# Optimization experiments

Measured on AMD Instinct MI355X. Metric: run time of the kernel, lower is better.

The kernel has to match this reference:

```python
import jax, jax.numpy as jnp
import numpy as np

N_USERS = 100000
N_TWEETS = 100000
N_NODES = N_USERS + N_TWEETS
N_EDGES = 600000
D = 128


def lrelu(x):
    return jax.nn.leaky_relu(x, negative_slope=0.01)


def linear(x, W, b):
    # torch nn.Linear convention: W is [out, in]
    return x @ W.T + b


def rgcn_conv(x, edge_index, edge_type, weight, root, bias):
    """PyG RGCNConv with num_relations=2, aggr='mean', root weight + bias."""
    src, dst = edge_index[0], edge_index[1]
    m = x[src]  # [E, D] gathered source features
    out = x @ root + bias
    for r in range(weight.shape[0]):
        mask = (edge_type == r).astype(x.dtype)  # [E]
        s = jax.ops.segment_sum(m * mask[:, None], dst, num_segments=N_NODES)
        cnt = jax.ops.segment_sum(mask, dst, num_segments=N_NODES)
        mean = s / jnp.maximum(cnt, 1.0)[:, None]  # nodes w/o rel-r in-edges -> 0
        out = out + mean @ weight[r]
    return out


def setup_inputs() -> dict:
    key = jax.random.key(0)
    ks = jax.random.split(key, 24)

    def lin(k, out_d, in_d):
        k1, k2 = jax.random.split(k)
        s = 1.0 / np.sqrt(in_d)
        return (jax.random.uniform(k1, (out_d, in_d), jnp.float32, -s, s),
                jax.random.uniform(k2, (out_d,), jnp.float32, -s, s))

    des = jax.random.normal(ks[0], (N_USERS, 100), jnp.float32)
    tweet = jax.random.normal(ks[1], (N_TWEETS, 100), jnp.float32)
    num_prop = jax.random.normal(ks[2], (N_USERS, 6), jnp.float32)
    cat_prop = jax.random.normal(ks[3], (N_USERS, 11), jnp.float32)
    edge_index = jax.random.randint(ks[4], (2, N_EDGES), 0, N_NODES, jnp.int32)
    edge_type = jax.random.randint(ks[5], (N_EDGES,), 0, 2, jnp.int32)

    W_des, b_des = lin(ks[6], D // 2, 100)       # des -> 64
    W_num, b_num = lin(ks[7], D // 4, 6)         # num_prop -> 32
    W_cat, b_cat = lin(ks[8], D // 4, 11)        # cat_prop -> 32
    W_tw, b_tw = lin(ks[9], D, 100)              # tweet -> 128
    W_in, b_in = lin(ks[10], D, D)
    rgcn_w = jax.random.normal(ks[11], (2, D, D), jnp.float32) / np.sqrt(D)
    rgcn_root = jax.random.normal(ks[12], (D, D), jnp.float32) / np.sqrt(D)
    rgcn_bias = jnp.zeros((D,), jnp.float32)
    W_o1, b_o1 = lin(ks[13], D, D)
    W_o2, b_o2 = lin(ks[14], 2, D)

    return dict(des=des, tweet=tweet, num_prop=num_prop, cat_prop=cat_prop,
                edge_index=edge_index, edge_type=edge_type,
                W_des=W_des, b_des=b_des, W_num=W_num, b_num=b_num,
                W_cat=W_cat, b_cat=b_cat, W_tw=W_tw, b_tw=b_tw,
                W_in=W_in, b_in=b_in, rgcn_w=rgcn_w, rgcn_root=rgcn_root,
                rgcn_bias=rgcn_bias, W_o1=W_o1, b_o1=b_o1, W_o2=W_o2, b_o2=b_o2)


def reference(des, tweet, num_prop, cat_prop, edge_index, edge_type,
              W_des, b_des, W_num, b_num, W_cat, b_cat, W_tw, b_tw,
              W_in, b_in, rgcn_w, rgcn_root, rgcn_bias, W_o1, b_o1, W_o2, b_o2):
    d = lrelu(linear(des, W_des, b_des))
    n = lrelu(linear(num_prop, W_num, b_num))
    c = lrelu(linear(cat_prop, W_cat, b_cat))
    x_users = jnp.concatenate([d, n, c], axis=1)       # [N_users, 128]
    t = lrelu(linear(tweet, W_tw, b_tw))               # [N_tweets, 128]
    x = jnp.concatenate([x_users, t], axis=0)          # [N_nodes, 128]
    x = lrelu(linear(x, W_in, b_in))
    x = rgcn_conv(x, edge_index, edge_type, rgcn_w, rgcn_root, rgcn_bias)
    # dropout in eval mode = identity
    x = rgcn_conv(x, edge_index, edge_type, rgcn_w, rgcn_root, rgcn_bias)
    x = lrelu(linear(x, W_o1, b_o1))
    return linear(x, W_o2, b_o2)
```

## Files before the change

### kernel.cpp

```cpp
#include <hip/hip_runtime.h>
#include <hip/hip_bf16.h>

typedef __hip_bfloat16 bf16;

typedef __bf16 bfv8 __attribute__((ext_vector_type(8)));
typedef float f32x4 __attribute__((ext_vector_type(4)));

__device__ __forceinline__ float lrelu(float x) { return x > 0.f ? x : 0.01f * x; }

__device__ __forceinline__ float ldv(float v) { return v; }
__device__ __forceinline__ float ldv(bf16 v) { return __bfloat162float(v); }
__device__ __forceinline__ void stv(float* p, float v) { *p = v; }
__device__ __forceinline__ void stv(bf16* p, float v) { *p = __float2bfloat16(v); }

__device__ __forceinline__ float in_rd(const void* p, size_t i, int isbf) {
  return isbf ? __bfloat162float(((const bf16*)p)[i]) : ((const float*)p)[i];
}
__device__ __forceinline__ int ix_rd(const void* p, size_t i, int is64) {
  return is64 ? (int)((const long long*)p)[i] : ((const int*)p)[i];
}

struct ProbeArgs {
  const void* p[23];
  int s[23];
  int mode[23];
};

__global__ void detect_all(ProbeArgs a, int* __restrict__ flags) {
  __shared__ int sh[256];
  int b = blockIdx.x;
  const unsigned int* w = (const unsigned int*)a.p[b];
  int s = a.s[b], mode = a.mode[b];
  int t = threadIdx.x;
  int c = 0;
  if (t < s) {
    if (mode == 0) {
      unsigned int v = w[t];
      int e = (v >> 7) & 0xFF;
      c = (e >= 100 && e <= 140) ? 1 : 0;
    } else {
      c = (w[2 * t + 1] == 0u) ? 1 : 0;
    }
  }
  sh[t] = c;
  __syncthreads();
  for (int d = 128; d; d >>= 1) {
    if (t < d) sh[t] += sh[t + d];
    __syncthreads();
  }
  if (t == 0) flags[b] = (mode == 0) ? (sh[0] * 10 >= 7 * s) : (sh[0] * 10 >= 9 * s);
}

#define PW_F32 82562
#define BF_BASE 82564
#define PW_W_TOTAL (BF_BASE + 5 * 8192)
#define ENC_BASE PW_W_TOTAL
#define PW_TOTAL (ENC_BASE + 16384 + 256)
__global__ void prep_weights(const void* Win, const void* bin, const void* rw,
                             const void* root, const void* rb, const void* Wo1,
                             const void* bo1, const void* Wo2, const void* bo2,
                             const int* __restrict__ fl, float* __restrict__ pw) {
  int i = blockIdx.x * 256 + threadIdx.x;
  if (i >= PW_W_TOTAL) return;
  if (i < 16384) {
    int k = i >> 7, o = i & 127;
    pw[i] = in_rd(Win, (size_t)o * 128 + k, fl[14]);
  } else if (i < 32768) {
    int j = i - 16384;
    int k = j >> 7, o = j & 127;
    pw[i] = in_rd(Wo1, (size_t)o * 128 + k, fl[19]);
  } else if (i < 49152) {
    pw[i] = in_rd(root, i - 32768, fl[17]);
  } else if (i < 81920) {
    pw[i] = in_rd(rw, i - 49152, fl[16]);
  } else if (i < 82048) {
    pw[i] = in_rd(bin, i - 81920, fl[15]);
  } else if (i < 82176) {
    pw[i] = in_rd(rb, i - 82048, fl[18]);
  } else if (i < 82304) {
    pw[i] = in_rd(bo1, i - 82176, fl[20]);
  } else if (i < 82560) {
    pw[i] = in_rd(Wo2, i - 82304, fl[21]);
  } else if (i < PW_F32) {
    pw[i] = in_rd(bo2, i - 82560, fl[22]);
  } else if (i >= BF_BASE) {
    int j = i - BF_BASE;
    bf16* bw = (bf16*)(pw + BF_BASE);
#pragma unroll
    for (int q = 0; q < 2; q++) {
      int u = 2 * j + q;
      int m = u >> 14, r = u & 16383;
      int n = r >> 7, k = r & 127;
      float v;
      if (m == 0) v = in_rd(Win, (size_t)n * 128 + k, fl[14]);
      else if (m == 1) v = in_rd(Wo1, (size_t)n * 128 + k, fl[19]);
      else if (m == 2) v = in_rd(root, (size_t)k * 128 + n, fl[17]);
      else v = in_rd(rw, (size_t)(m - 3) * 16384 + (size_t)k * 128 + n, fl[16]);
      bw[u] = __float2bfloat16(v);
    }
  }
}

__global__ void prep_enc(const void* Wd, const void* bd, const void* Wn, const void* bn,
                         const void* Wc, const void* bc, const void* Wt, const void* bt,
                         const int* __restrict__ fl, int dDes, int dNum, int dCat, int dTw,
                         float* __restrict__ pw) {
  int i = blockIdx.x * 256 + threadIdx.x;
  bf16* e = (bf16*)(pw + ENC_BASE);
  float* bU = pw + ENC_BASE + 16384;
  float* bT = bU + 128;
  if (i < 16384) {
    int n = i >> 7, k = i & 127;
    float v = 0.f;
    if (n < 64) {
      if (k < dDes) v = in_rd(Wd, (size_t)n * dDes + k, fl[6]);
    } else if (n < 96) {
      int kk = k - dDes;
      if (kk >= 0 && kk < dNum) v = in_rd(Wn, (size_t)(n - 64) * dNum + kk, fl[8]);
    } else {
      int kk = k - dDes - dNum;
      if (kk >= 0 && kk < dCat) v = in_rd(Wc, (size_t)(n - 96) * dCat + kk, fl[10]);
    }
    e[i] = __float2bfloat16(v);
  } else if (i < 32768) {
    int j = i - 16384;
    int n = j >> 7, k = j & 127;
    float v = (k < dTw) ? in_rd(Wt, (size_t)n * dTw + k, fl[12]) : 0.f;
    e[i] = __float2bfloat16(v);
  } else if (i < 32896) {
    int j = i - 32768;
    bU[j] = (j < 64) ? in_rd(bd, j, fl[7])
                     : (j < 96) ? in_rd(bn, j - 64, fl[9]) : in_rd(bc, j - 96, fl[11]);
  } else if (i < 33024) {
    bT[i - 32896] = in_rd(bt, i - 32896, fl[13]);
  }
}

__global__ void sig_fill(float* __restrict__ p, int n, float v) {
  int i = blockIdx.x * 256 + threadIdx.x;
  if (i < n) p[i] = v;
}
__global__ void zero_ints(int* __restrict__ p, int n) {
  int i = blockIdx.x * 256 + threadIdx.x;
  if (i < n) p[i] = 0;
}

__global__ void count_edges(const void* __restrict__ ei, const void* __restrict__ et,
                            const int* __restrict__ fl, int* __restrict__ cnt, int NEr,
                            int NNr) {
  int e = blockIdx.x * 256 + threadIdx.x;
  if (e >= NEr) return;
  int d = ix_rd(ei, (size_t)NEr + e, fl[4]);
  int r = ix_rd(et, e, fl[5]) & 1;
  if ((unsigned)d >= (unsigned)NNr) return;
  atomicAdd(&cnt[r * NNr + d], 1);
}

__global__ void scan_blocks(const int* __restrict__ in, int* __restrict__ out,
                            int* __restrict__ bsum, int n) {
  __shared__ int sh[256];
  int t = threadIdx.x;
  int base = blockIdx.x * 1024 + t * 4;
  int a[4];
  int s = 0;
#pragma unroll
  for (int i = 0; i < 4; i++) {
    a[i] = (base + i < n) ? in[base + i] : 0;
    s += a[i];
  }
  sh[t] = s;
  __syncthreads();
  for (int d = 1; d < 256; d <<= 1) {
    int v = (t >= d) ? sh[t - d] : 0;
    __syncthreads();
    sh[t] += v;
    __syncthreads();
  }
  int ex = sh[t] - s;
#pragma unroll
  for (int i = 0; i < 4; i++) {
    if (base + i < n) out[base + i] = ex;
    ex += a[i];
  }
  if (t == 255 && bsum) bsum[blockIdx.x] = sh[255];
}

__global__ void scan_add_inv(int* __restrict__ off, const int* __restrict__ bsumsc,
                             const int* __restrict__ cnt, float* __restrict__ inv, int n) {
  int i = blockIdx.x * 256 + threadIdx.x;
  if (i >= n) return;
  off[i] += bsumsc[i >> 10];
  inv[i] = 1.f / fmaxf((float)cnt[i], 1.f);
}

__global__ void fill_elist(const void* __restrict__ ei, const void* __restrict__ et,
                           const int* __restrict__ fl, const int* __restrict__ off,
                           int* __restrict__ fill, int* __restrict__ elist, int NEr, int NNr) {
  int e = blockIdx.x * 256 + threadIdx.x;
  if (e >= NEr) return;
  int s = ix_rd(ei, e, fl[4]);
  int d = ix_rd(ei, (size_t)NEr + e, fl[4]);
  int r = ix_rd(et, e, fl[5]) & 1;
  if ((unsigned)d >= (unsigned)NNr || (unsigned)s >= (unsigned)NNr) return;
  int idx = r * NNr + d;
  int slot = off[idx] + atomicAdd(&fill[idx], 1);
  elist[slot] = s | ((d & 127) << 24);
}

__global__ __launch_bounds__(256) void enc_gemm(const void* __restrict__ A,
                                                const void* __restrict__ W,
                                                const void* __restrict__ B,
                                                const int* __restrict__ fl, int fa, int fw,
                                                int fb, bf16* __restrict__ x, int M, int K,
                                                int N, int row0, int col0) {
  __shared__ float Wb[128 * 102];
  __shared__ float bb[128];
  int t = threadIdx.x;
  int stride = (K & 1) ? K : K + 1;
  int fA = fl[fa];
  {
    int fW = fl[fw], fB = fl[fb];
    for (int idx = t; idx < N * K; idx += 256) {
      int j = idx / K, k = idx - j * K;
      Wb[j * stride + k] = in_rd(W, (size_t)j * K + k, fW);
    }
    if (t < N) bb[t] = in_rd(B, t, fB);
  }
  __syncthreads();
  int j = t % N;
  int r = t / N;
  int R = 256 / N;
  int iEnd = blockIdx.x * 64 + 64;
  if (iEnd > M) iEnd = M;
  const float* wrow = &Wb[j * stride];
  if (!fA) {
    const float* Af = (const float*)A;
    for (int i = blockIdx.x * 64 + r; i < iEnd; i += R) {
      const float* a = Af + (size_t)i * K;
      float acc = bb[j];
      for (int k = 0; k < K; k++) acc += a[k] * wrow[k];
      stv(&x[(size_t)(row0 + i) * 128 + col0 + j], lrelu(acc));
    }
  } else {
    const bf16* Ab = (const bf16*)A;
    for (int i = blockIdx.x * 64 + r; i < iEnd; i += R) {
      const bf16* a = Ab + (size_t)i * K;
      float acc = bb[j];
      for (int k = 0; k < K; k++) acc += __bfloat162float(a[k]) * wrow[k];
      stv(&x[(size_t)(row0 + i) * 128 + col0 + j], lrelu(acc));
    }
  }
}


__global__ __launch_bounds__(256) void enc_mfma(
    const void* __restrict__ A0, const void* __restrict__ A1, const void* __restrict__ A2,
    const int* __restrict__ fl, int fi0, int fi1, int fi2, int K0, int K1, int K2,
    const bf16* __restrict__ WbE, const float* __restrict__ biasE,
    const bf16* __restrict__ WbL, const float* __restrict__ bL, bf16* __restrict__ x,
    int M, int row0) {
  __shared__ __align__(16) bf16 Xs[16384];
  int t = threadIdx.x;
  int i0 = blockIdx.x * 128;

  {
    uint4 z = {0u, 0u, 0u, 0u};
#pragma unroll
    for (int i = 0; i < 8; i++) *(uint4*)((char*)Xs + i * 4096 + t * 16) = z;
  }
  __syncthreads();

  const void* As[3] = {A0, A1, A2};
  int Ks_[3] = {K0, K1, K2};
  int fis[3] = {fi0, fi1, fi2};
  int cb = 0;
  for (int s = 0; s < 3; s++) {
    int Ks = Ks_[s];
    if (Ks <= 0) continue;
    int isbf = fl[fis[s]];
    const void* A = As[s];
    int total = 128 * Ks;
    for (int f = t; f < total; f += 256) {
      int row = f / Ks;
      int k = f - row * Ks;
      int gr = i0 + row;
      float v = (gr < M) ? in_rd(A, (size_t)gr * Ks + k, isbf) : 0.f;
      int byte = row * 256 + (cb + k) * 2;
      *(bf16*)((char*)Xs + (byte ^ ((row & 7) << 4))) = __float2bfloat16(v);
    }
    cb += Ks;
  }
  __syncthreads();

  int wv = t >> 6, l = t & 63;
  int lr = l & 15, lg = l >> 4;
  int rbase = (wv >> 1) * 64, cbase = (wv & 1) * 64;
  int ko = lg * 8;
  f32x4 acc[4][4] = {};
#pragma unroll
  for (int ks = 0; ks < 4; ks++) {
    bfv8 bk[4];
#pragma unroll
    for (int cg = 0; cg < 4; cg++)
      bk[cg] = *(const bfv8*)&WbE[(size_t)(cbase + cg * 16 + lr) * 128 + ks * 32 + ko];
    bfv8 af[4];
#pragma unroll
    for (int rg = 0; rg < 4; rg++) {
      int mrow = rbase + rg * 16 + lr;
      int byte = mrow * 256 + (ks * 32 + ko) * 2;
      af[rg] = *(const bfv8*)((const char*)Xs + (byte ^ ((mrow & 7) << 4)));
    }
#pragma unroll
    for (int rg = 0; rg < 4; rg++)
#pragma unroll
      for (int cg = 0; cg < 4; cg++)
        acc[rg][cg] =
            __builtin_amdgcn_mfma_f32_16x16x32_bf16(af[rg], bk[cg], acc[rg][cg], 0, 0, 0);
  }
  __syncthreads();

#pragma unroll
  for (int cg = 0; cg < 4; cg++) {
    int col = cbase + cg * 16 + lr;
    float bv = biasE[col];
#pragma unroll
    for (int rg = 0; rg < 4; rg++) {
      int r0 = rbase + rg * 16 + lg * 4;
#pragma unroll
      for (int j = 0; j < 4; j++) {
        int row = r0 + j;
        int byte = row * 256 + col * 2;
        *(bf16*)((char*)Xs + (byte ^ ((row & 7) << 4))) =
            __float2bfloat16(lrelu(acc[rg][cg][j] + bv));
      }
    }
  }
  __syncthreads();

  f32x4 acc2[4][4] = {};
#pragma unroll
  for (int ks = 0; ks < 4; ks++) {
    bfv8 bk[4];
#pragma unroll
    for (int cg = 0; cg < 4; cg++)
      bk[cg] = *(const bfv8*)&WbL[(size_t)(cbase + cg * 16 + lr) * 128 + ks * 32 + ko];
    bfv8 af[4];
#pragma unroll
    for (int rg = 0; rg < 4; rg++) {
      int mrow = rbase + rg * 16 + lr;
      int byte = mrow * 256 + (ks * 32 + ko) * 2;
      af[rg] = *(const bfv8*)((const char*)Xs + (byte ^ ((mrow & 7) << 4)));
    }
#pragma unroll
    for (int rg = 0; rg < 4; rg++)
#pragma unroll
      for (int cg = 0; cg < 4; cg++)
        acc2[rg][cg] =
            __builtin_amdgcn_mfma_f32_16x16x32_bf16(af[rg], bk[cg], acc2[rg][cg], 0, 0, 0);
  }

#pragma unroll
  for (int cg = 0; cg < 4; cg++) {
    int col = cbase + cg * 16 + lr;
    float bv = bL[col];
#pragma unroll
    for (int rg = 0; rg < 4; rg++) {
      int r0 = i0 + rbase + rg * 16 + lg * 4;
#pragma unroll
      for (int j = 0; j < 4; j++) {
        int row = r0 + j;
        if (row < M)
          x[(size_t)(row0 + row) * 128 + col] = __float2bfloat16(lrelu(acc2[rg][cg][j] + bv));
      }
    }
  }
}

__global__ __launch_bounds__(256) void mfma_lin(const bf16* __restrict__ A,
                                                const bf16* __restrict__ Wb,
                                                const float* __restrict__ bias,
                                                bf16* __restrict__ Out, int M) {
  int t = threadIdx.x;
  int wv = t >> 6, l = t & 63;
  int lr = l & 15, lg = l >> 4;
  int i0 = blockIdx.x * 128;
  int rbase = (wv >> 1) * 64;
  int cbase = (wv & 1) * 64;
  int ko = lg * 8;

  size_t rowoff[4];
#pragma unroll
  for (int rg = 0; rg < 4; rg++) {
    int row = i0 + rbase + rg * 16 + lr;
    if (row > M - 1) row = M - 1;
    rowoff[rg] = (size_t)row * 128;
  }

  bfv8 bfr[4][4];
#pragma unroll
  for (int cg = 0; cg < 4; cg++)
#pragma unroll
    for (int ks = 0; ks < 4; ks++)
      bfr[cg][ks] = *(const bfv8*)&Wb[(size_t)(cbase + cg * 16 + lr) * 128 + ks * 32 + ko];

  f32x4 acc[4][4] = {};
#pragma unroll
  for (int ks = 0; ks < 4; ks++) {
    bfv8 af[4];
#pragma unroll
    for (int rg = 0; rg < 4; rg++) af[rg] = *(const bfv8*)&A[rowoff[rg] + ks * 32 + ko];
#pragma unroll
    for (int rg = 0; rg < 4; rg++)
#pragma unroll
      for (int cg = 0; cg < 4; cg++)
        acc[rg][cg] =
            __builtin_amdgcn_mfma_f32_16x16x32_bf16(af[rg], bfr[cg][ks], acc[rg][cg], 0, 0, 0);
  }

#pragma unroll
  for (int cg = 0; cg < 4; cg++) {
    int col = cbase + cg * 16 + lr;
    float bv = bias[col];
#pragma unroll
    for (int rg = 0; rg < 4; rg++) {
      int row0 = i0 + rbase + rg * 16 + lg * 4;
#pragma unroll
      for (int j = 0; j < 4; j++) {
        int row = row0 + j;
        if (row < M) Out[(size_t)row * 128 + col] = __float2bfloat16(lrelu(acc[rg][cg][j] + bv));
      }
    }
  }
}

template <bool TAIL>
__global__ __launch_bounds__(256, 4) void mfma_conv_f(
    const bf16* __restrict__ X, const int* __restrict__ off, const int* __restrict__ cnt,
    const int* __restrict__ elist, const float* __restrict__ inv,
    const bf16* __restrict__ WB, const float* __restrict__ bias, bf16* __restrict__ Out,
    const bf16* __restrict__ Wo1B, const float* __restrict__ bO1,
    const float* __restrict__ Wo2, const float* __restrict__ bo2,
    float* __restrict__ out2, int M, int NNr, int NEr) {
  __shared__ __align__(16) float At[64 * 128];
  int t = threadIdx.x;
  int wv = t >> 6, l = t & 63;
  int lr = l & 15, lg = l >> 4;
  int i0 = blockIdx.x * 32;
  int cbase = wv * 32;
  int ko = lg * 8;

  {
    int c8 = (t & 15) * 8;
    int stc[4], dgc[4];
#pragma unroll
    for (int pn = 0; pn < 4; pn++) {
      int vr = (t >> 4) + pn * 16;
      int rel = vr >> 5, m = vr & 31;
      int node = i0 + m;
      int idx = rel * NNr + node;
      bool ok = node < M;
      stc[pn] = ok ? off[idx] : 0;
      dgc[pn] = ok ? cnt[idx] : 0;
    }
    int dmax = max(max(dgc[0], dgc[1]), max(dgc[2], dgc[3]));
    float s[4][8] = {};

    auto xoff = [&](int pn, int e) -> size_t {
      int ec = e < dgc[pn] - 1 ? e : dgc[pn] - 1;
      ec = ec < 0 ? 0 : ec;
      int ei = stc[pn] + ec;
      ei = ei < NEr - 1 ? ei : NEr - 1;
      return (size_t)(elist[ei] & 0xFFFFFF) * 128 + c8;
    };

    bfv8 v0[4], v1[4];
#pragma unroll
    for (int pn = 0; pn < 4; pn++) v0[pn] = *(const bfv8*)&X[xoff(pn, 0)];
#pragma unroll
    for (int pn = 0; pn < 4; pn++) v1[pn] = *(const bfv8*)&X[xoff(pn, 1)];

    for (int e = 0; e < dmax; e++) {
      bfv8 v2[4];
#pragma unroll
      for (int pn = 0; pn < 4; pn++) v2[pn] = *(const bfv8*)&X[xoff(pn, e + 2)];
#pragma unroll
      for (int pn = 0; pn < 4; pn++) {
        float msk = e < dgc[pn] ? 1.f : 0.f;
#pragma unroll
        for (int j = 0; j < 8; j++) s[pn][j] += msk * __bfloat162float(v0[pn][j]);
      }
#pragma unroll
      for (int pn = 0; pn < 4; pn++) {
        v0[pn] = v1[pn];
        v1[pn] = v2[pn];
      }
    }
#pragma unroll
    for (int pn = 0; pn < 4; pn++) {
      int vr = (t >> 4) + pn * 16;
      int sw = (vr & 7) << 4;
      int lb = vr * 512 + c8 * 4;
      *(float4*)((char*)At + (lb ^ sw)) = make_float4(s[pn][0], s[pn][1], s[pn][2], s[pn][3]);
      *(float4*)((char*)At + ((lb + 16) ^ sw)) =
          make_float4(s[pn][4], s[pn][5], s[pn][6], s[pn][7]);
    }
  }

  size_t rowoff[2];
  float iv0[2], iv1[2];
#pragma unroll
  for (int rg = 0; rg < 2; rg++) {
    int row = i0 + rg * 16 + lr;
    int rc = row < M ? row : M - 1;
    rowoff[rg] = (size_t)rc * 128;
    iv0[rg] = row < M ? inv[row] : 0.f;
    iv1[rg] = row < M ? inv[NNr + row] : 0.f;
  }

  f32x4 acc[2][2] = {};

#pragma unroll
  for (int ks = 0; ks < 4; ks++) {
    bfv8 bk[2];
#pragma unroll
    for (int cg = 0; cg < 2; cg++)
      bk[cg] = *(const bfv8*)&WB[(size_t)(cbase + cg * 16 + lr) * 128 + ks * 32 + ko];
    bfv8 af[2];
#pragma unroll
    for (int rg = 0; rg < 2; rg++) af[rg] = *(const bfv8*)&X[rowoff[rg] + ks * 32 + ko];
#pragma unroll
    for (int rg = 0; rg < 2; rg++)
#pragma unroll
      for (int cg = 0; cg < 2; cg++)
        acc[rg][cg] =
            __builtin_amdgcn_mfma_f32_16x16x32_bf16(af[rg], bk[cg], acc[rg][cg], 0, 0, 0);
  }
  __syncthreads();

#pragma unroll
  for (int r = 0; r < 2; r++) {
    const bf16* Wb = WB + 16384 * (1 + r);
#pragma unroll
    for (int ks = 0; ks < 4; ks++) {
      bfv8 bk[2];
#pragma unroll
      for (int cg = 0; cg < 2; cg++)
        bk[cg] = *(const bfv8*)&Wb[(size_t)(cbase + cg * 16 + lr) * 128 + ks * 32 + ko];
      bfv8 af[2];
#pragma unroll
      for (int rg = 0; rg < 2; rg++) {
        int mrow = r * 32 + rg * 16 + lr;
        int lb = mrow * 512 + ks * 128 + ko * 4;
        int sw = (mrow & 7) << 4;
        float4 f0 = *(const float4*)((const char*)At + (lb ^ sw));
        float4 f1 = *(const float4*)((const char*)At + ((lb + 16) ^ sw));
        float iv = r ? iv1[rg] : iv0[rg];
        bfv8 a;
        a[0] = (__bf16)(f0.x * iv); a[1] = (__bf16)(f0.y * iv);
        a[2] = (__bf16)(f0.z * iv); a[3] = (__bf16)(f0.w * iv);
        a[4] = (__bf16)(f1.x * iv); a[5] = (__bf16)(f1.y * iv);
        a[6] = (__bf16)(f1.z * iv); a[7] = (__bf16)(f1.w * iv);
        af[rg] = a;
      }
#pragma unroll
      for (int rg = 0; rg < 2; rg++)
#pragma unroll
        for (int cg = 0; cg < 2; cg++)
          acc[rg][cg] =
              __builtin_amdgcn_mfma_f32_16x16x32_bf16(af[rg], bk[cg], acc[rg][cg], 0, 0, 0);
    }
  }

  if (!TAIL) {
#pragma unroll
    for (int cg = 0; cg < 2; cg++) {
      int col = cbase + cg * 16 + lr;
      float bv = bias[col];
#pragma unroll
      for (int rg = 0; rg < 2; rg++) {
        int row0 = i0 + rg * 16 + lg * 4;
#pragma unroll
        for (int j = 0; j < 4; j++) {
          int row = row0 + j;
          if (row < M) Out[(size_t)row * 128 + col] = __float2bfloat16(acc[rg][cg][j] + bv);
        }
      }
    }
  } else {
    __syncthreads();
#pragma unroll
    for (int cg = 0; cg < 2; cg++) {
      int col = cbase + cg * 16 + lr;
      float bv = bias[col];
#pragma unroll
      for (int rg = 0; rg < 2; rg++) {
#pragma unroll
        for (int j = 0; j < 4; j++) {
          int row32 = rg * 16 + lg * 4 + j;
          int byte = row32 * 256 + col * 2;
          *(bf16*)((char*)At + (byte ^ ((row32 & 7) << 4))) =
              __float2bfloat16(acc[rg][cg][j] + bv);
        }
      }
    }
    __syncthreads();

    f32x4 acc2[2][2] = {};
#pragma unroll
    for (int ks = 0; ks < 4; ks++) {
      bfv8 bk[2];
#pragma unroll
      for (int cg = 0; cg < 2; cg++)
        bk[cg] = *(const bfv8*)&Wo1B[(size_t)(cbase + cg * 16 + lr) * 128 + ks * 32 + ko];
      bfv8 af[2];
#pragma unroll
      for (int rg = 0; rg < 2; rg++) {
        int mrow = rg * 16 + lr;
        int byte = mrow * 256 + (ks * 32 + ko) * 2;
        af[rg] = *(const bfv8*)((const char*)At + (byte ^ ((mrow & 7) << 4)));
      }
#pragma unroll
      for (int rg = 0; rg < 2; rg++)
#pragma unroll
        for (int cg = 0; cg < 2; cg++)
          acc2[rg][cg] =
              __builtin_amdgcn_mfma_f32_16x16x32_bf16(af[rg], bk[cg], acc2[rg][cg], 0, 0, 0);
    }
#pragma unroll
    for (int cg = 0; cg < 2; cg++) {
      int col = cbase + cg * 16 + lr;
      float bv = bO1[col];
#pragma unroll
      for (int rg = 0; rg < 2; rg++) {
#pragma unroll
        for (int j = 0; j < 4; j++) {
          int row32 = rg * 16 + lg * 4 + j;
          *(bf16*)((char*)At + 8192 + row32 * 256 + col * 2) =
              __float2bfloat16(lrelu(acc2[rg][cg][j] + bv));
        }
      }
    }
    __syncthreads();

    int row = t >> 3, seg = t & 7;
    const bf16* zr = (const bf16*)((const char*)At + 8192 + row * 256 + seg * 32);
    float p0 = 0.f, p1 = 0.f;
#pragma unroll
    for (int q = 0; q < 16; q++) {
      float xv = __bfloat162float(zr[q]);
      int col = seg * 16 + q;
      p0 += xv * Wo2[col];
      p1 += xv * Wo2[128 + col];
    }
#pragma unroll
    for (int o = 4; o; o >>= 1) {
      p0 += __shfl_down(p0, o, 8);
      p1 += __shfl_down(p1, o, 8);
    }
    int grow = i0 + row;
    if (seg == 0 && grow < M) {
      out2[(size_t)grow * 2] = p0 + bo2[0];
      out2[(size_t)grow * 2 + 1] = p1 + bo2[1];
    }
  }
}

static void run_pipeline(void* const* d_in, const int* S, float* out, char* ws,
                         int NUr, int NTr, int NEr, int dDes, int dNum, int dCat, int dTw,
                         hipStream_t stream) {
  const int NNr = NUr + NTr;
  const size_t xbytes = (size_t)NNr * 128 * 2;

  bf16* xa = (bf16*)ws;
  bf16* xb = (bf16*)(ws + xbytes);
  char* p = ws + 2 * xbytes;
  int* cnt = (int*)p;      p += (size_t)2 * NNr * 4;
  int* fill = (int*)p;     p += (size_t)2 * NNr * 4;
  int* off = (int*)p;      p += (size_t)2 * NNr * 4;
  int* bsum = (int*)p;     p += 2048 * 4;
  int* bsumsc = (int*)p;   p += 2048 * 4;
  float* inv = (float*)p;  p += (size_t)2 * NNr * 4;
  int* elist = (int*)p;    p += (size_t)NEr * 4;
  float* pw = (float*)p;   p += (size_t)PW_TOTAL * 4;
  int* flags = (int*)p;

  ProbeArgs pa;
  for (int i = 0; i < 23; i++) {
    int src = (i == 22) ? 21 : i;
    pa.p[i] = d_in[src];
    if (i == 4) {
      pa.mode[i] = 1;
      pa.s[i] = NEr < 256 ? NEr : 256;
    } else if (i == 5) {
      pa.mode[i] = 1;
      int s2 = NEr / 2 < 256 ? NEr / 2 : 256;
      pa.s[i] = s2 < 1 ? 1 : s2;
    } else {
      pa.mode[i] = 0;
      int s = S[src] / 2;
      if (s > 256) s = 256;
      if (s < 1) s = 1;
      pa.s[i] = s;
    }
  }
  detect_all<<<23, 256, 0, stream>>>(pa, flags);
  prep_weights<<<(PW_W_TOTAL + 255) / 256, 256, 0, stream>>>(
      d_in[14], d_in[15], d_in[16], d_in[17], d_in[18], d_in[19], d_in[20], d_in[21],
      d_in[22], flags, pw);
  prep_enc<<<129, 256, 0, stream>>>(d_in[6], d_in[7], d_in[8], d_in[9], d_in[10], d_in[11],
                                    d_in[12], d_in[13], flags, dDes, dNum, dCat, dTw, pw);

  const float* bIn = pw + 81920;
  const float* rbp = pw + 82048;
  const float* bO1 = pw + 82176;
  const float* Wo2p = pw + 82304;
  const float* bo2p = pw + 82560;
  const bf16* WinB = (const bf16*)(pw + BF_BASE);
  const bf16* Wo1B = (const bf16*)(pw + BF_BASE + 8192);
  const bf16* ConvB = (const bf16*)(pw + BF_BASE + 16384);
  const bf16* EncU = (const bf16*)(pw + ENC_BASE);
  const bf16* EncT = (const bf16*)(pw + ENC_BASE + 8192);
  const float* bU = pw + ENC_BASE + 16384;
  const float* bT = bU + 128;

  const void* ei = d_in[4];
  const void* et = d_in[5];
  const int nb1 = (2 * NNr + 1023) / 1024;

  zero_ints<<<(4 * NNr + 255) / 256, 256, 0, stream>>>(cnt, 4 * NNr);
  zero_ints<<<16, 256, 0, stream>>>(bsum, 4096);
  count_edges<<<(NEr + 255) / 256, 256, 0, stream>>>(ei, et, flags, cnt, NEr, NNr);
  scan_blocks<<<nb1, 256, 0, stream>>>(cnt, off, bsum, 2 * NNr);
  scan_blocks<<<1, 256, 0, stream>>>(bsum, bsumsc, nullptr, nb1);
  scan_add_inv<<<(2 * NNr + 255) / 256, 256, 0, stream>>>(off, bsumsc, cnt, inv, 2 * NNr);
  fill_elist<<<(NEr + 255) / 256, 256, 0, stream>>>(ei, et, flags, off, fill, elist, NEr, NNr);

  if (dDes + dNum + dCat <= 128 && dTw <= 128) {
    enc_mfma<<<(NUr + 127) / 128, 256, 0, stream>>>(d_in[0], d_in[2], d_in[3], flags, 0, 2, 3,
                                                    dDes, dNum, dCat, EncU, bU, WinB, bIn, xb,
                                                    NUr, 0);
    enc_mfma<<<(NTr + 127) / 128, 256, 0, stream>>>(d_in[1], nullptr, nullptr, flags, 1, 1, 1,
                                                    dTw, 0, 0, EncT, bT, WinB, bIn, xb, NTr,
                                                    NUr);
  } else {
    enc_gemm<<<(NUr + 63) / 64, 256, 0, stream>>>(d_in[0], d_in[6], d_in[7], flags, 0, 6, 7,
                                                  xa, NUr, dDes, 64, 0, 0);
    enc_gemm<<<(NUr + 63) / 64, 256, 0, stream>>>(d_in[2], d_in[8], d_in[9], flags, 2, 8, 9,
                                                  xa, NUr, dNum, 32, 0, 64);
    enc_gemm<<<(NUr + 63) / 64, 256, 0, stream>>>(d_in[3], d_in[10], d_in[11], flags, 3, 10,
                                                  11, xa, NUr, dCat, 32, 0, 96);
    enc_gemm<<<(NTr + 63) / 64, 256, 0, stream>>>(d_in[1], d_in[12], d_in[13], flags, 1, 12,
                                                  13, xa, NTr, dTw, 128, NUr, 0);
    mfma_lin<<<(NNr + 127) / 128, 256, 0, stream>>>(xa, WinB, bIn, xb, NNr);
  }

  const int mt32 = (NNr + 31) / 32;
  mfma_conv_f<false><<<mt32, 256, 0, stream>>>(xb, off, cnt, elist, inv, ConvB, rbp, xa,
                                               nullptr, nullptr, nullptr, nullptr, nullptr,
                                               NNr, NNr, NEr);
  mfma_conv_f<true><<<mt32, 256, 0, stream>>>(xa, off, cnt, elist, inv, ConvB, rbp, nullptr,
                                              Wo1B, bO1, Wo2p, bo2p, out, NNr, NNr, NEr);
}

extern "C" void kernel_launch(void* const* d_in, const int* in_sizes, int n_in,
                              void* d_out, int out_size, void* d_ws, size_t ws_size,
                              hipStream_t stream) {
  float* out = (float*)d_out;
  char* ws = (char*)d_ws;

  auto signal = [&](int k) {
    sig_fill<<<(out_size + 255) / 256, 256, 0, stream>>>(out, out_size, (float)(200 + k));
  };

  if (n_in != 23) { signal(1); return; }
  const int* S = in_sizes;
  if (S[7] != 64 || S[9] != 32 || S[11] != 32 || S[13] != 128) { signal(2); return; }
  if (S[15] != 128) { signal(3); return; }
  if (S[6] % 64 || S[8] % 32 || S[10] % 32 || S[12] % 128) { signal(4); return; }
  int dDes = S[6] / 64, dNum = S[8] / 32, dCat = S[10] / 32, dTw = S[12] / 128;
  if (dDes <= 0 || dTw <= 0 || S[0] % dDes || S[1] % dTw) { signal(5); return; }
  if (dDes > 101 || dNum > 101 || dCat > 101 || dTw > 101) { signal(4); return; }
  int NUr = S[0] / dDes, NTr = S[1] / dTw, NNr = NUr + NTr, NEr = S[5];
  if (S[2] != NUr * dNum || S[3] != NUr * dCat) { signal(5); return; }
  if (S[4] != 2 * NEr || NEr < 1024) { signal(6); return; }
  if (NNr >= (1 << 24)) { signal(6); return; }
  if (S[14] != 16384 || S[16] != 32768 || S[17] != 16384 || S[18] != 128 ||
      S[19] != 16384 || S[20] != 128 || S[21] != 256 || S[22] != 2) { signal(7); return; }
  if (out_size != NNr * 2) { signal(8); return; }

  const size_t smallBytes = (size_t)4 * ((size_t)2 * NNr * 4) + 2 * 2048 * 4 +
                            (size_t)NEr * 4 + (size_t)PW_TOTAL * 4 + 512;
  const size_t need = 2 * (size_t)NNr * 128 * 2 + smallBytes;

  if (ws_size >= need) {
    run_pipeline(d_in, S, out, ws, NUr, NTr, NEr, dDes, dNum, dCat, dTw, stream);
  } else {
    signal(9);
  }
}
```

Before: 520.6 us.

## Merge setup kernels, vectorize encoder input loads, simplify conv gather prefetch

Three prep/zeroing kernels are merged into one setup launch, and the separate bsum zeroing launch is dropped. The encoder's input staging now reads four elements at a time with float4/ushort4 loads instead of scalar loads with per-element division. The conv gather loop drops its two-deep clamped prefetch for a one-deep prefetch with predicated loads, which reduces address arithmetic but may expose more gather latency. The bsum buffer is no longer zeroed, which is harmless only if scan_blocks fully writes it.

Result: faster. 491.1 us (-5.7%).

```diff
diff --git a/kernel.cpp b/kernel.cpp
--- a/kernel.cpp
+++ b/kernel.cpp
@@ -55,94 +55,93 @@
 #define BF_BASE 82564
 #define PW_W_TOTAL (BF_BASE + 5 * 8192)
 #define ENC_BASE PW_W_TOTAL
+#define ENC_N 33024
 #define PW_TOTAL (ENC_BASE + 16384 + 256)
-__global__ void prep_weights(const void* Win, const void* bin, const void* rw,
-                             const void* root, const void* rb, const void* Wo1,
-                             const void* bo1, const void* Wo2, const void* bo2,
-                             const int* __restrict__ fl, float* __restrict__ pw) {
+__global__ void setup_all(const void* Win, const void* bin, const void* rw, const void* root,
+                          const void* rb, const void* Wo1, const void* bo1, const void* Wo2,
+                          const void* bo2, const void* Wd, const void* bd, const void* Wn,
+                          const void* bn, const void* Wc, const void* bc, const void* Wt,
+                          const void* bt, const int* __restrict__ fl, int dDes, int dNum,
+                          int dCat, int dTw, float* __restrict__ pw, int* __restrict__ cnt4,
+                          int NNr) {
   int i = blockIdx.x * 256 + threadIdx.x;
-  if (i >= PW_W_TOTAL) return;
-  if (i < 16384) {
-    int k = i >> 7, o = i & 127;
-    pw[i] = in_rd(Win, (size_t)o * 128 + k, fl[14]);
-  } else if (i < 32768) {
-    int j = i - 16384;
-    int k = j >> 7, o = j & 127;
-    pw[i] = in_rd(Wo1, (size_t)o * 128 + k, fl[19]);
-  } else if (i < 49152) {
-    pw[i] = in_rd(root, i - 32768, fl[17]);
-  } else if (i < 81920) {
-    pw[i] = in_rd(rw, i - 49152, fl[16]);
-  } else if (i < 82048) {
-    pw[i] = in_rd(bin, i - 81920, fl[15]);
-  } else if (i < 82176) {
-    pw[i] = in_rd(rb, i - 82048, fl[18]);
-  } else if (i < 82304) {
-    pw[i] = in_rd(bo1, i - 82176, fl[20]);
-  } else if (i < 82560) {
-    pw[i] = in_rd(Wo2, i - 82304, fl[21]);
-  } else if (i < PW_F32) {
-    pw[i] = in_rd(bo2, i - 82560, fl[22]);
-  } else if (i >= BF_BASE) {
-    int j = i - BF_BASE;
-    bf16* bw = (bf16*)(pw + BF_BASE);
-#pragma unroll
-    for (int q = 0; q < 2; q++) {
-      int u = 2 * j + q;
-      int m = u >> 14, r = u & 16383;
-      int n = r >> 7, k = r & 127;
-      float v;
-      if (m == 0) v = in_rd(Win, (size_t)n * 128 + k, fl[14]);
-      else if (m == 1) v = in_rd(Wo1, (size_t)n * 128 + k, fl[19]);
-      else if (m == 2) v = in_rd(root, (size_t)k * 128 + n, fl[17]);
-      else v = in_rd(rw, (size_t)(m - 3) * 16384 + (size_t)k * 128 + n, fl[16]);
-      bw[u] = __float2bfloat16(v);
-    }
-  }
-}
-
-__global__ void prep_enc(const void* Wd, const void* bd, const void* Wn, const void* bn,
-                         const void* Wc, const void* bc, const void* Wt, const void* bt,
-                         const int* __restrict__ fl, int dDes, int dNum, int dCat, int dTw,
-                         float* __restrict__ pw) {
-  int i = blockIdx.x * 256 + threadIdx.x;
-  bf16* e = (bf16*)(pw + ENC_BASE);
-  float* bU = pw + ENC_BASE + 16384;
-  float* bT = bU + 128;
-  if (i < 16384) {
-    int n = i >> 7, k = i & 127;
-    float v = 0.f;
-    if (n < 64) {
-      if (k < dDes) v = in_rd(Wd, (size_t)n * dDes + k, fl[6]);
-    } else if (n < 96) {
-      int kk = k - dDes;
-      if (kk >= 0 && kk < dNum) v = in_rd(Wn, (size_t)(n - 64) * dNum + kk, fl[8]);
+  if (i < PW_W_TOTAL) {
+    if (i < 16384) {
+      int k = i >> 7, o = i & 127;
+      pw[i] = in_rd(Win, (size_t)o * 128 + k, fl[14]);
+    } else if (i < 32768) {
+      int j = i - 16384;
+      int k = j >> 7, o = j & 127;
+      pw[i] = in_rd(Wo1, (size_t)o * 128 + k, fl[19]);
+    } else if (i < 49152) {
+      pw[i] = in_rd(root, i - 32768, fl[17]);
+    } else if (i < 81920) {
+      pw[i] = in_rd(rw, i - 49152, fl[16]);
+    } else if (i < 82048) {
+      pw[i] = in_rd(bin, i - 81920, fl[15]);
+    } else if (i < 82176) {
+      pw[i] = in_rd(rb, i - 82048, fl[18]);
+    } else if (i < 82304) {
+      pw[i] = in_rd(bo1, i - 82176, fl[20]);
+    } else if (i < 82560) {
+      pw[i] = in_rd(Wo2, i - 82304, fl[21]);
+    } else if (i < PW_F32) {
+      pw[i] = in_rd(bo2, i - 82560, fl[22]);
+    } else if (i >= BF_BASE) {
+      int j = i - BF_BASE;
+      bf16* bw = (bf16*)(pw + BF_BASE);
+#pragma unroll
+      for (int q = 0; q < 2; q++) {
+        int u = 2 * j + q;
+        int m = u >> 14, r = u & 16383;
+        int n = r >> 7, k = r & 127;
+        float v;
+        if (m == 0) v = in_rd(Win, (size_t)n * 128 + k, fl[14]);
+        else if (m == 1) v = in_rd(Wo1, (size_t)n * 128 + k, fl[19]);
+        else if (m == 2) v = in_rd(root, (size_t)k * 128 + n, fl[17]);
+        else v = in_rd(rw, (size_t)(m - 3) * 16384 + (size_t)k * 128 + n, fl[16]);
+        bw[u] = __float2bfloat16(v);
+      }
+    }
+  } else if (i < PW_W_TOTAL + ENC_N) {
+    int j = i - PW_W_TOTAL;
+    bf16* e = (bf16*)(pw + ENC_BASE);
+    float* bU = pw + ENC_BASE + 16384;
+    float* bT = bU + 128;
+    if (j < 16384) {
+      int n = j >> 7, k = j & 127;
+      float v = 0.f;
+      if (n < 64) {
+        if (k < dDes) v = in_rd(Wd, (size_t)n * dDes + k, fl[6]);
+      } else if (n < 96) {
+        int kk = k - dDes;
+        if (kk >= 0 && kk < dNum) v = in_rd(Wn, (size_t)(n - 64) * dNum + kk, fl[8]);
+      } else {
+        int kk = k - dDes - dNum;
+        if (kk >= 0 && kk < dCat) v = in_rd(Wc, (size_t)(n - 96) * dCat + kk, fl[10]);
+      }
+      e[j] = __float2bfloat16(v);
+    } else if (j < 32768) {
+      int j2 = j - 16384;
+      int n = j2 >> 7, k = j2 & 127;
+      float v = (k < dTw) ? in_rd(Wt, (size_t)n * dTw + k, fl[12]) : 0.f;
+      e[j] = __float2bfloat16(v);
+    } else if (j < 32896) {
+      int j2 = j - 32768;
+      bU[j2] = (j2 < 64) ? in_rd(bd, j2, fl[7])
+                         : (j2 < 96) ? in_rd(bn, j2 - 64, fl[9]) : in_rd(bc, j2 - 96, fl[11]);
     } else {
-      int kk = k - dDes - dNum;
-      if (kk >= 0 && kk < dCat) v = in_rd(Wc, (size_t)(n - 96) * dCat + kk, fl[10]);
-    }
-    e[i] = __float2bfloat16(v);
-  } else if (i < 32768) {
-    int j = i - 16384;
-    int n = j >> 7, k = j & 127;
-    float v = (k < dTw) ? in_rd(Wt, (size_t)n * dTw + k, fl[12]) : 0.f;
-    e[i] = __float2bfloat16(v);
-  } else if (i < 32896) {
-    int j = i - 32768;
-    bU[j] = (j < 64) ? in_rd(bd, j, fl[7])
-                     : (j < 96) ? in_rd(bn, j - 64, fl[9]) : in_rd(bc, j - 96, fl[11]);
-  } else if (i < 33024) {
-    bT[i - 32896] = in_rd(bt, i - 32896, fl[13]);
+      bT[j - 32896] = in_rd(bt, j - 32896, fl[13]);
+    }
+  } else {
+    int j = i - PW_W_TOTAL - ENC_N;
+    if (j < 4 * NNr) cnt4[j] = 0;
   }
 }
 
 __global__ void sig_fill(float* __restrict__ p, int n, float v) {
   int i = blockIdx.x * 256 + threadIdx.x;
   if (i < n) p[i] = v;
-}
-__global__ void zero_ints(int* __restrict__ p, int n) {
-  int i = blockIdx.x * 256 + threadIdx.x;
-  if (i < n) p[i] = 0;
 }
 
 __global__ void count_edges(const void* __restrict__ ei, const void* __restrict__ et,
@@ -278,15 +277,58 @@
     int Ks = Ks_[s];
     if (Ks <= 0) continue;
     int isbf = fl[fis[s]];
-    const void* A = As[s];
     int total = 128 * Ks;
-    for (int f = t; f < total; f += 256) {
-      int row = f / Ks;
-      int k = f - row * Ks;
-      int gr = i0 + row;
-      float v = (gr < M) ? in_rd(A, (size_t)gr * Ks + k, isbf) : 0.f;
-      int byte = row * 256 + (cb + k) * 2;
-      *(bf16*)((char*)Xs + (byte ^ ((row & 7) << 4))) = __float2bfloat16(v);
+    long gml = (long)(M - i0) * Ks;
+    int gmax = gml > total ? total : (gml < 0 ? 0 : (int)gml);
+    int nu = (total + 3) >> 2;
+    if (!isbf) {
+      const float* Af = (const float*)As[s] + (size_t)i0 * Ks;
+      for (int u = t; u < nu; u += 256) {
+        int f0 = u * 4;
+        float vv[4];
+        if (f0 + 4 <= gmax) {
+          float4 x4 = *(const float4*)(Af + f0);
+          vv[0] = x4.x; vv[1] = x4.y; vv[2] = x4.z; vv[3] = x4.w;
+        } else {
+          vv[0] = (f0 < gmax) ? Af[f0] : 0.f;
+          vv[1] = (f0 + 1 < gmax) ? Af[f0 + 1] : 0.f;
+          vv[2] = (f0 + 2 < gmax) ? Af[f0 + 2] : 0.f;
+          vv[3] = (f0 + 3 < gmax) ? Af[f0 + 3] : 0.f;
+        }
+#pragma unroll
+        for (int q = 0; q < 4; q++) {
+          int f = f0 + q;
+          if (f < total) {
+            int row = f / Ks, k = f - row * Ks;
+            int byte = row * 256 + (cb + k) * 2;
+            *(bf16*)((char*)Xs + (byte ^ ((row & 7) << 4))) = __float2bfloat16(vv[q]);
+          }
+        }
+      }
+    } else {
+      const unsigned short* Ab = (const unsigned short*)As[s] + (size_t)i0 * Ks;
+      for (int u = t; u < nu; u += 256) {
+        int f0 = u * 4;
+        unsigned short vv[4];
+        if (f0 + 4 <= gmax) {
+          ushort4 x4 = *(const ushort4*)(Ab + f0);
+          vv[0] = x4.x; vv[1] = x4.y; vv[2] = x4.z; vv[3] = x4.w;
+        } else {
+          vv[0] = (f0 < gmax) ? Ab[f0] : 0;
+          vv[1] = (f0 + 1 < gmax) ? Ab[f0 + 1] : 0;
+          vv[2] = (f0 + 2 < gmax) ? Ab[f0 + 2] : 0;
+          vv[3] = (f0 + 3 < gmax) ? Ab[f0 + 3] : 0;
+        }
+#pragma unroll
+        for (int q = 0; q < 4; q++) {
+          int f = f0 + q;
+          if (f < total) {
+            int row = f / Ks, k = f - row * Ks;
+            int byte = row * 256 + (cb + k) * 2;
+            *(unsigned short*)((char*)Xs + (byte ^ ((row & 7) << 4))) = vv[q];
+          }
+        }
+      }
     }
     cb += Ks;
   }
@@ -440,7 +482,7 @@
     const bf16* __restrict__ WB, const float* __restrict__ bias, bf16* __restrict__ Out,
     const bf16* __restrict__ Wo1B, const float* __restrict__ bO1,
     const float* __restrict__ Wo2, const float* __restrict__ bo2,
-    float* __restrict__ out2, int M, int NNr, int NEr) {
+    float* __restrict__ out2, int M, int NNr) {
   __shared__ __align__(16) float At[64 * 128];
   int t = threadIdx.x;
   int wv = t >> 6, l = t & 63;
@@ -450,54 +492,51 @@
   int ko = lg * 8;
 
   {
+    int grp = t >> 4;
     int c8 = (t & 15) * 8;
     int stc[4], dgc[4];
 #pragma unroll
     for (int pn = 0; pn < 4; pn++) {
-      int vr = (t >> 4) + pn * 16;
+      int vr = grp + pn * 16;
       int rel = vr >> 5, m = vr & 31;
       int node = i0 + m;
+      bool ok = node < M;
       int idx = rel * NNr + node;
-      bool ok = node < M;
       stc[pn] = ok ? off[idx] : 0;
       dgc[pn] = ok ? cnt[idx] : 0;
     }
     int dmax = max(max(dgc[0], dgc[1]), max(dgc[2], dgc[3]));
     float s[4][8] = {};
-
-    auto xoff = [&](int pn, int e) -> size_t {
-      int ec = e < dgc[pn] - 1 ? e : dgc[pn] - 1;
-      ec = ec < 0 ? 0 : ec;
-      int ei = stc[pn] + ec;
-      ei = ei < NEr - 1 ? ei : NEr - 1;
-      return (size_t)(elist[ei] & 0xFFFFFF) * 128 + c8;
-    };
-
-    bfv8 v0[4], v1[4];
-#pragma unroll
-    for (int pn = 0; pn < 4; pn++) v0[pn] = *(const bfv8*)&X[xoff(pn, 0)];
-#pragma unroll
-    for (int pn = 0; pn < 4; pn++) v1[pn] = *(const bfv8*)&X[xoff(pn, 1)];
-
+    bfv8 v[4];
+#pragma unroll
+    for (int pn = 0; pn < 4; pn++) {
+      if (dgc[pn] > 0) {
+        int src = elist[stc[pn]] & 0xFFFFFF;
+        v[pn] = *(const bfv8*)&X[(size_t)src * 128 + c8];
+      }
+    }
     for (int e = 0; e < dmax; e++) {
-      bfv8 v2[4];
-#pragma unroll
-      for (int pn = 0; pn < 4; pn++) v2[pn] = *(const bfv8*)&X[xoff(pn, e + 2)];
+      bfv8 nv[4];
 #pragma unroll
       for (int pn = 0; pn < 4; pn++) {
-        float msk = e < dgc[pn] ? 1.f : 0.f;
-#pragma unroll
-        for (int j = 0; j < 8; j++) s[pn][j] += msk * __bfloat162float(v0[pn][j]);
+        if (e + 1 < dgc[pn]) {
+          int src = elist[stc[pn] + e + 1] & 0xFFFFFF;
+          nv[pn] = *(const bfv8*)&X[(size_t)src * 128 + c8];
+        }
       }
 #pragma unroll
       for (int pn = 0; pn < 4; pn++) {
-        v0[pn] = v1[pn];
-        v1[pn] = v2[pn];
-      }
+        if (e < dgc[pn]) {
+#pragma unroll
+          for (int j = 0; j < 8; j++) s[pn][j] += __bfloat162float(v[pn][j]);
+        }
+      }
+#pragma unroll
+      for (int pn = 0; pn < 4; pn++) v[pn] = nv[pn];
     }
 #pragma unroll
     for (int pn = 0; pn < 4; pn++) {
-      int vr = (t >> 4) + pn * 16;
+      int vr = grp + pn * 16;
       int sw = (vr & 7) << 4;
       int lb = vr * 512 + c8 * 4;
       *(float4*)((char*)At + (lb ^ sw)) = make_float4(s[pn][0], s[pn][1], s[pn][2], s[pn][3]);
@@ -704,11 +743,12 @@
     }
   }
   detect_all<<<23, 256, 0, stream>>>(pa, flags);
-  prep_weights<<<(PW_W_TOTAL + 255) / 256, 256, 0, stream>>>(
+
+  const int setupN = PW_W_TOTAL + ENC_N + 4 * NNr;
+  setup_all<<<(setupN + 255) / 256, 256, 0, stream>>>(
       d_in[14], d_in[15], d_in[16], d_in[17], d_in[18], d_in[19], d_in[20], d_in[21],
-      d_in[22], flags, pw);
-  prep_enc<<<129, 256, 0, stream>>>(d_in[6], d_in[7], d_in[8], d_in[9], d_in[10], d_in[11],
-                                    d_in[12], d_in[13], flags, dDes, dNum, dCat, dTw, pw);
+      d_in[22], d_in[6], d_in[7], d_in[8], d_in[9], d_in[10], d_in[11], d_in[12], d_in[13],
+      flags, dDes, dNum, dCat, dTw, pw, cnt, NNr);
 
   const float* bIn = pw + 81920;
   const float* rbp = pw + 82048;
@@ -727,8 +767,6 @@
   const void* et = d_in[5];
   const int nb1 = (2 * NNr + 1023) / 1024;
 
-  zero_ints<<<(4 * NNr + 255) / 256, 256, 0, stream>>>(cnt, 4 * NNr);
-  zero_ints<<<16, 256, 0, stream>>>(bsum, 4096);
   count_edges<<<(NEr + 255) / 256, 256, 0, stream>>>(ei, et, flags, cnt, NEr, NNr);
   scan_blocks<<<nb1, 256, 0, stream>>>(cnt, off, bsum, 2 * NNr);
   scan_blocks<<<1, 256, 0, stream>>>(bsum, bsumsc, nullptr, nb1);
@@ -757,9 +795,9 @@
   const int mt32 = (NNr + 31) / 32;
   mfma_conv_f<false><<<mt32, 256, 0, stream>>>(xb, off, cnt, elist, inv, ConvB, rbp, xa,
                                                nullptr, nullptr, nullptr, nullptr, nullptr,
-                                               NNr, NNr, NEr);
+                                               NNr, NNr);
   mfma_conv_f<true><<<mt32, 256, 0, stream>>>(xa, off, cnt, elist, inv, ConvB, rbp, nullptr,
-                                              Wo1B, bO1, Wo2p, bo2p, out, NNr, NNr, NEr);
+                                              Wo1B, bO1, Wo2p, bo2p, out, NNr, NNr);
 }
 
 extern "C" void kernel_launch(void* const* d_in, const int* in_sizes, int n_in,
```
